# Kernel optimization log

Hardware: AMD Instinct MI355X
Metric: run time of the kernel (lower is better)

Reference implementation:

```python
import jax, jax.numpy as jnp
import numpy as np

B, S, D = 2, 2048, 1024   # batch, seq, in_shape
H, E = 16, 64             # num_heads, out_shape (per-head dim)

def setup_inputs() -> dict:
    key = jax.random.key(0)
    ks = jax.random.split(key, 5)
    x = jax.random.normal(ks[0], (B, S, D), dtype=jnp.float32)
    Wq = jax.random.normal(ks[1], (H, D, E), dtype=jnp.float32) * 0.02
    Wk = jax.random.normal(ks[2], (H, D, E), dtype=jnp.float32) * 0.02
    Wv = jax.random.normal(ks[3], (H, D, E), dtype=jnp.float32) * 0.02
    W = jax.random.normal(ks[4], (H * E, E), dtype=jnp.float32) * 0.02
    return {"x": x, "Wq": Wq, "Wk": Wk, "Wv": Wv, "W": W}

def reference(x, Wq, Wk, Wv, W):
    # Per-head projections (stacked over heads): [B,H,S,E]
    q = jnp.einsum("bsd,hde->bhse", x, Wq)
    k = jnp.einsum("bsd,hde->bhse", x, Wk)
    v = jnp.einsum("bsd,hde->bhse", x, Wv)
    scale = 1.0 / jnp.sqrt(jnp.float32(E))
    # Full causal scores [B,H,S,S] with -inf above diagonal (as in original)
    scores = jnp.einsum("bhse,bhte->bhst", q, k) * scale
    causal = jnp.tril(jnp.ones((S, S), dtype=bool))
    scores = jnp.where(causal, scores, -jnp.inf)
    attn = jax.nn.softmax(scores, axis=-1)
    ctx = jnp.einsum("bhst,bhte->bhse", attn, v)          # [B,H,S,E]
    # concat heads along last dim (head-major order matches tf.concat over list)
    ctx = jnp.transpose(ctx, (0, 2, 1, 3)).reshape(B, S, H * E)
    return ctx @ W                                         # [B,S,E]
```

## Files before the change

kernel.cpp:

```cpp
#include <hip/hip_runtime.h>
#include <hip/hip_bf16.h>
#include <cstdint>
#include <cstddef>

#define BB 2
#define SS 2048
#define DD 1024
#define HH 16
#define EE 64

typedef short bf16x8 __attribute__((ext_vector_type(8)));
typedef short s4 __attribute__((ext_vector_type(4)));
typedef float f32x4 __attribute__((ext_vector_type(4)));
typedef float float4v __attribute__((ext_vector_type(4)));
typedef unsigned int u32x2 __attribute__((ext_vector_type(2)));

#define GLDS(gp, lp) __builtin_amdgcn_global_load_lds( \
    (const __attribute__((address_space(1))) void*)(gp), \
    (__attribute__((address_space(3))) void*)(lp), 16, 0, 0)

static __device__ __forceinline__ short f2bf(float f) {
    union { float f; uint32_t u; } v; v.f = f;
    uint32_t r = (v.u + 0x7fffu + ((v.u >> 16) & 1u)) >> 16;
    return (short)r;
}

static __device__ __forceinline__ uint32_t cvtpk(float a, float b) {
    uint32_t r;
    asm("v_cvt_pk_bf16_f32 %0, %1, %2" : "=v"(r) : "v"(a), "v"(b));
    return r;
}

__global__ __launch_bounds__(256) void prep_kernel(const float* __restrict__ x,
                                                   const float* __restrict__ Wq,
                                                   const float* __restrict__ Wk,
                                                   const float* __restrict__ Wv,
                                                   const float* __restrict__ W,
                                                   short* __restrict__ xb,
                                                   short* __restrict__ wt,
                                                   short* __restrict__ wot) {
    __shared__ float tile[64][65];
    int blk = blockIdx.x;
    int t = threadIdx.x;
    if (blk < 4096) {
        int i = blk * 256 + t;
        float4v v = ((const float4v*)x)[i];
        s4 o; o[0] = f2bf(v[0]); o[1] = f2bf(v[1]); o[2] = f2bf(v[2]); o[3] = f2bf(v[3]);
        ((s4*)xb)[i] = o;
        return;
    }
    int idx = blk - 4096;
    const float* src;
    short* d;
    int R, r0;
    if (idx < 768) {
        int bx = idx & 15, by = idx >> 4;
        int which = by >> 4, mtx = by & 15;
        src = ((which == 0) ? Wq : (which == 1) ? Wk : Wv) + (size_t)mtx * DD * 64;
        d = wt + (size_t)which * HH * EE * DD + (size_t)mtx * DD * 64;
        R = DD; r0 = bx * 64;
    } else {
        int bx = idx - 768;
        src = W; d = wot; R = HH * EE; r0 = bx * 64;
    }
#pragma unroll
    for (int i = 0; i < 16; ++i) {
        int id2 = t + i * 256;
        int r = id2 >> 6, c = id2 & 63;
        tile[r][c] = src[(size_t)(r0 + r) * 64 + c];
    }
    __syncthreads();
#pragma unroll
    for (int i = 0; i < 16; ++i) {
        int id2 = t + i * 256;
        int e = id2 >> 6, dd2 = id2 & 63;
        d[(size_t)e * R + r0 + dd2] = f2bf(tile[dd2][e]);
    }
}

__global__ __launch_bounds__(256, 3) void qkv_gemm(const short* __restrict__ A,
                                                   const short* __restrict__ Bt,
                                                   short* __restrict__ Qo,
                                                   short* __restrict__ Ko,
                                                   short* __restrict__ Vto) {
    __shared__ __align__(16) short As3[3][64 * 64];
    __shared__ __align__(16) short Bs3[3][64 * 64];
    int tid = threadIdx.x;
    int wv = tid >> 6, lane = tid & 63;
    int m = lane & 15, g = lane >> 4;
    int wr = wv >> 1, wc = wv & 1;

    int xcd = blockIdx.x & 7, idx = blockIdx.x >> 3;
    int mb = (xcd & 3) * 8 + (idx & 7);
    int nb = (xcd >> 2) * 12 + (idx >> 3);
    int rowBase = mb * 128, colBase0 = nb * 128;

    int src_row[2], src_kcol[2];
#pragma unroll
    for (int j = 0; j < 2; ++j) {
        int si = j * 256 + tid;
        int sr = si >> 3, sp = si & 7;
        int sl = sp ^ (sr & 7);
        src_row[j] = 2 * sr + (sl >> 2);
        src_kcol[j] = (sl & 3) * 8;
    }
    const short* aP0 = A + (size_t)(rowBase + src_row[0]) * DD + src_kcol[0];
    const short* aP1 = A + (size_t)(rowBase + src_row[1]) * DD + src_kcol[1];
    const short* bP0 = Bt + (size_t)(colBase0 + src_row[0]) * DD + src_kcol[0];
    const short* bP1 = Bt + (size_t)(colBase0 + src_row[1]) * DD + src_kcol[1];
    int dst0 = (wv * 64) * 8;
    int dst1 = (256 + wv * 64) * 8;

    f32x4 acc[4][4];
#pragma unroll
    for (int i = 0; i < 4; ++i)
#pragma unroll
        for (int j = 0; j < 4; ++j) acc[i][j] = {0, 0, 0, 0};

    int rdoff = ((m & 1) * 64 + g * 16) ^ (((m >> 1) & 7) << 4);
    int mh = m >> 1;

    auto STAGE = [&](int buf, int kt) {
        short* ab = &As3[buf][0];
        short* bb = &Bs3[buf][0];
        GLDS(aP0 + kt, ab + dst0);
        GLDS(aP1 + kt, ab + dst1);
        GLDS(bP0 + kt, bb + dst0);
        GLDS(bP1 + kt, bb + dst1);
    };

    auto COMPUTE = [&](int buf) {
        bf16x8 af[4], bfr[4];
#pragma unroll
        for (int mi = 0; mi < 4; ++mi)
            af[mi] = *(const bf16x8*)((const char*)&As3[buf][(wr * 32 + mi * 8 + mh) * 64] + rdoff);
#pragma unroll
        for (int ni = 0; ni < 4; ++ni)
            bfr[ni] = *(const bf16x8*)((const char*)&Bs3[buf][(wc * 32 + ni * 8 + mh) * 64] + rdoff);
        asm volatile("s_waitcnt lgkmcnt(0)\ns_barrier" ::: "memory");
        __builtin_amdgcn_s_setprio(1);
#pragma unroll
        for (int mi = 0; mi < 4; ++mi)
#pragma unroll
            for (int ni = 0; ni < 4; ++ni)
                acc[mi][ni] = __builtin_amdgcn_mfma_f32_16x16x32_bf16(af[mi], bfr[ni], acc[mi][ni], 0, 0, 0);
        __builtin_amdgcn_s_setprio(0);
    };

    STAGE(0, 0);
    STAGE(1, 32);
    for (int t = 0; t < 30; ++t) {
        STAGE((t + 2) % 3, (t + 2) * 32);
        asm volatile("s_waitcnt vmcnt(8)\ns_barrier" ::: "memory");
        COMPUTE(t % 3);
    }
    asm volatile("s_waitcnt vmcnt(4)\ns_barrier" ::: "memory");
    COMPUTE(0);
    asm volatile("s_waitcnt vmcnt(0)\ns_barrier" ::: "memory");
    COMPUTE(1);

    int colw = colBase0 + wc * 64;
    int mtx = colw >> 10;
    int h = (colw >> 6) & 15;
    int rb = rowBase + wr * 64;

    if (mtx == 0) {
        const float qs = 0.125f * 1.44269504089f;
#pragma unroll
        for (int mi = 0; mi < 4; ++mi)
#pragma unroll
            for (int ni = 0; ni < 4; ++ni)
#pragma unroll
                for (int r = 0; r < 4; ++r) {
                    int row = rb + mi * 16 + g * 4 + r;
                    int b = row >> 11, s = row & 2047;
                    Qo[((size_t)(b * HH + h) * SS + s) * EE + ni * 16 + m] = f2bf(acc[mi][ni][r] * qs);
                }
    } else if (mtx == 1) {
#pragma unroll
        for (int mi = 0; mi < 4; ++mi)
#pragma unroll
            for (int ni = 0; ni < 4; ++ni)
#pragma unroll
                for (int r = 0; r < 4; ++r) {
                    int row = rb + mi * 16 + g * 4 + r;
                    int b = row >> 11, s = row & 2047;
                    Ko[((size_t)(b * HH + h) * SS + s) * EE + ni * 16 + m] = f2bf(acc[mi][ni][r]);
                }
    } else {
#pragma unroll
        for (int mi = 0; mi < 4; ++mi)
#pragma unroll
            for (int ni = 0; ni < 4; ++ni) {
                int row0 = rb + mi * 16 + g * 4;
                int b = row0 >> 11, s = row0 & 2047;
                s4 o; o[0] = f2bf(acc[mi][ni][0]); o[1] = f2bf(acc[mi][ni][1]);
                o[2] = f2bf(acc[mi][ni][2]); o[3] = f2bf(acc[mi][ni][3]);
                *(s4*)&Vto[((size_t)(b * HH + h) * EE + ni * 16 + m) * SS + s] = o;
            }
    }
}

__global__ __launch_bounds__(256, 4) void attn_kernel(const short* __restrict__ Q,
                                                      const short* __restrict__ K,
                                                      const short* __restrict__ Vt,
                                                      short* __restrict__ ctx) {
    __shared__ __align__(16) short Ks[2][64 * 64];
    __shared__ __align__(16) short Vs[2][64 * 64];
    __shared__ __align__(16) short pl[4][1024];
    int tid = threadIdx.x;
    int wv = tid >> 6, lane = tid & 63;
    int m = lane & 15, g = lane >> 4;
    int xcd = blockIdx.x & 7, i = blockIdx.x >> 3;
    int bh = xcd * 4 + (i & 3);
    int qblk = 31 - (i >> 2);
    int b = bh >> 4, h = bh & 15;
    const short* Qb = Q + (size_t)bh * SS * EE;
    const short* Kb = K + (size_t)bh * SS * EE;
    const short* Vb = Vt + (size_t)bh * EE * SS;
    int qrow = qblk * 64 + wv * 16 + m;

    int srow = wv * 8 + (lane >> 3);
    int scol_s = (((lane & 7) * 16) ^ ((srow & 7) << 4)) >> 1;

    bf16x8 qa0 = *(const bf16x8*)(Qb + (size_t)qrow * EE + g * 8);
    bf16x8 qa1 = *(const bf16x8*)(Qb + (size_t)qrow * EE + 32 + g * 8);

    int sw = (m & 7) << 4;
    int c0 = (g * 16) ^ sw;
    int c1 = (64 + g * 16) ^ sw;
    char* plrow = (char*)&pl[wv][0] + m * 128;

    float mreg = -INFINITY, lsum = 0.f;
    f32x4 o[4];
#pragma unroll
    for (int n = 0; n < 4; ++n) { o[n][0] = 0.f; o[n][1] = 0.f; o[n][2] = 0.f; o[n][3] = 0.f; }

    auto STAGE = [&](int nb, int t0) {
        short* kd = &Ks[0][0] + nb * 4096 + wv * 512;
        short* vd = &Vs[0][0] + nb * 4096 + wv * 512;
        const short* ksrc = Kb + (size_t)(t0 + srow) * EE + scol_s;
        const short* vsrc = Vb + (size_t)srow * SS + t0 + scol_s;
        GLDS(ksrc, kd);
        GLDS(ksrc + 32 * EE, kd + 2048);
        GLDS(vsrc, vd);
        GLDS(vsrc + (size_t)32 * SS, vd + 2048);
    };

    int ntile = qblk + 1;
    STAGE(0, 0);
    __syncthreads();

    for (int tt = 0; tt < ntile; ++tt) {
        if (tt + 1 < ntile) STAGE((tt + 1) & 1, (tt + 1) * 64);
        int t0 = tt * 64;
        const short* Ksb = &Ks[0][0] + (tt & 1) * 4096;
        const short* Vsb = &Vs[0][0] + (tt & 1) * 4096;

        f32x4 sc[4] = {{0,0,0,0},{0,0,0,0},{0,0,0,0},{0,0,0,0}};
#pragma unroll
        for (int n = 0; n < 4; ++n) {
            const char* krow = (const char*)(Ksb + (n * 16 + m) * 64);
            bf16x8 kb0 = *(const bf16x8*)(krow + c0);
            sc[n] = __builtin_amdgcn_mfma_f32_16x16x32_bf16(kb0, qa0, sc[n], 0, 0, 0);
            bf16x8 kb1 = *(const bf16x8*)(krow + c1);
            sc[n] = __builtin_amdgcn_mfma_f32_16x16x32_bf16(kb1, qa1, sc[n], 0, 0, 0);
        }

        if (tt == qblk) {
#pragma unroll
            for (int n = 0; n < 4; ++n)
#pragma unroll
                for (int r = 0; r < 4; ++r)
                    if (t0 + n * 16 + g * 4 + r > qrow) sc[n][r] = -INFINITY;
        }

        float mx = sc[0][0];
#pragma unroll
        for (int n = 0; n < 4; ++n)
#pragma unroll
            for (int r = 0; r < 4; ++r) mx = fmaxf(mx, sc[n][r]);
        mx = fmaxf(mx, __shfl_xor(mx, 16, 64));
        mx = fmaxf(mx, __shfl_xor(mx, 32, 64));

        if (!__all(mx <= mreg + 11.5f)) {
            float mn = fmaxf(mreg, mx);
            float al = exp2f(mreg - mn);
            lsum *= al;
#pragma unroll
            for (int n = 0; n < 4; ++n)
#pragma unroll
                for (int r = 0; r < 4; ++r) o[n][r] *= al;
            mreg = mn;
        }

#pragma unroll
        for (int n = 0; n < 4; ++n) {
            float p0 = exp2f(sc[n][0] - mreg);
            float p1 = exp2f(sc[n][1] - mreg);
            float p2 = exp2f(sc[n][2] - mreg);
            float p3 = exp2f(sc[n][3] - mreg);
            lsum += (p0 + p1) + (p2 + p3);
            u32x2 pk; pk[0] = cvtpk(p0, p1); pk[1] = cvtpk(p2, p3);
            *(u32x2*)(plrow + ((n * 32 + g * 8) ^ sw)) = pk;
        }

#pragma unroll
        for (int ks = 0; ks < 2; ++ks) {
            int cv = ks ? c1 : c0;
            bf16x8 pa = *(const bf16x8*)(plrow + cv);
#pragma unroll
            for (int n = 0; n < 4; ++n) {
                const char* vrow = (const char*)(Vsb + (n * 16 + m) * 64);
                bf16x8 vb = *(const bf16x8*)(vrow + cv);
                o[n] = __builtin_amdgcn_mfma_f32_16x16x32_bf16(vb, pa, o[n], 0, 0, 0);
            }
        }

        __syncthreads();
    }

    lsum += __shfl_xor(lsum, 16, 64);
    lsum += __shfl_xor(lsum, 32, 64);
    float inv = 1.0f / lsum;
    short* cb = ctx + (size_t)(b * SS + qrow) * (HH * EE) + h * EE;
#pragma unroll
    for (int n = 0; n < 4; ++n) {
        u32x2 k0; k0[0] = cvtpk(o[n][0] * inv, o[n][1] * inv);
        k0[1] = cvtpk(o[n][2] * inv, o[n][3] * inv);
        *(u32x2*)&cb[n * 16 + g * 4] = k0;
    }
}

__global__ __launch_bounds__(256) void outproj_kernel(const short* __restrict__ ctx,
                                                      const short* __restrict__ wot,
                                                      float* __restrict__ out) {
    __shared__ float red[4][1024];
    int wv = threadIdx.x >> 6, lane = threadIdx.x & 63;
    int m = lane & 15, g = lane >> 4;
    int r0 = blockIdx.x * 16;
    const short* arow = ctx + (size_t)(r0 + m) * (HH * EE) + g * 8;
    const short* wb = wot + g * 8;
    f32x4 acc[4] = {{0,0,0,0},{0,0,0,0},{0,0,0,0},{0,0,0,0}};
    int k0 = wv * 256;
    for (int d0 = k0; d0 < k0 + 256; d0 += 32) {
        bf16x8 a = *(const bf16x8*)(arow + d0);
#pragma unroll
        for (int n = 0; n < 4; ++n) {
            bf16x8 bbf = *(const bf16x8*)(wb + (size_t)(n * 16 + m) * (HH * EE) + d0);
            acc[n] = __builtin_amdgcn_mfma_f32_16x16x32_bf16(a, bbf, acc[n], 0, 0, 0);
        }
    }
#pragma unroll
    for (int n = 0; n < 4; ++n)
#pragma unroll
        for (int r = 0; r < 4; ++r)
            red[wv][(g * 4 + r) * 64 + n * 16 + m] = acc[n][r];
    __syncthreads();
    int t = threadIdx.x;
    float4v sum = ((const float4v*)red[0])[t];
    sum += ((const float4v*)red[1])[t];
    sum += ((const float4v*)red[2])[t];
    sum += ((const float4v*)red[3])[t];
    ((float4v*)(out + (size_t)blockIdx.x * 1024))[t] = sum;
}

extern "C" void kernel_launch(void* const* d_in, const int* in_sizes, int n_in,
                              void* d_out, int out_size, void* d_ws, size_t ws_size,
                              hipStream_t stream) {
    const float* x  = (const float*)d_in[0];
    const float* Wq = (const float*)d_in[1];
    const float* Wk = (const float*)d_in[2];
    const float* Wv = (const float*)d_in[3];
    const float* W  = (const float*)d_in[4];
    float* out = (float*)d_out;

    char* w = (char*)d_ws;
    short* xb  = (short*)w;
    short* wqt = (short*)(w + ((size_t)8 << 20));
    short* wot = wqt + (size_t)3 * HH * EE * DD;
    short* Qb  = wot + (size_t)64 * 1024;
    short* Kb  = Qb + (size_t)BB * HH * SS * EE;
    short* Vtb = Kb + (size_t)BB * HH * SS * EE;
    short* ctx = Vtb + (size_t)BB * HH * SS * EE;

    prep_kernel<<<4880, 256, 0, stream>>>(x, Wq, Wk, Wv, W, xb, wqt, wot);
    qkv_gemm<<<768, 256, 0, stream>>>(xb, wqt, Qb, Kb, Vtb);
    attn_kernel<<<1024, 256, 0, stream>>>(Qb, Kb, Vtb, ctx);
    outproj_kernel<<<256, 256, 0, stream>>>(ctx, wot, out);
}
```

Measured before the change: 94.89 us.

## Keep softmax probabilities in registers by permuting K tile row layout

```diff
diff --git a/kernel.cpp b/kernel.cpp
--- a/kernel.cpp
+++ b/kernel.cpp
@@ -14,6 +14,7 @@
 typedef float f32x4 __attribute__((ext_vector_type(4)));
 typedef float float4v __attribute__((ext_vector_type(4)));
 typedef unsigned int u32x2 __attribute__((ext_vector_type(2)));
+typedef unsigned int u32x4 __attribute__((ext_vector_type(4)));
 
 #define GLDS(gp, lp) __builtin_amdgcn_global_load_lds( \
     (const __attribute__((address_space(1))) void*)(gp), \
@@ -201,13 +202,12 @@
     }
 }
 
-__global__ __launch_bounds__(256, 4) void attn_kernel(const short* __restrict__ Q,
+__global__ __launch_bounds__(256, 5) void attn_kernel(const short* __restrict__ Q,
                                                       const short* __restrict__ K,
                                                       const short* __restrict__ Vt,
                                                       short* __restrict__ ctx) {
     __shared__ __align__(16) short Ks[2][64 * 64];
     __shared__ __align__(16) short Vs[2][64 * 64];
-    __shared__ __align__(16) short pl[4][1024];
     int tid = threadIdx.x;
     int wv = tid >> 6, lane = tid & 63;
     int m = lane & 15, g = lane >> 4;
@@ -222,6 +222,7 @@
 
     int srow = wv * 8 + (lane >> 3);
     int scol_s = (((lane & 7) * 16) ^ ((srow & 7) << 4)) >> 1;
+    int trow = ((srow >> 4) & 1) * 32 + ((srow >> 2) & 3) * 8 + (srow & 3);
 
     bf16x8 qa0 = *(const bf16x8*)(Qb + (size_t)qrow * EE + g * 8);
     bf16x8 qa1 = *(const bf16x8*)(Qb + (size_t)qrow * EE + 32 + g * 8);
@@ -229,7 +230,6 @@
     int sw = (m & 7) << 4;
     int c0 = (g * 16) ^ sw;
     int c1 = (64 + g * 16) ^ sw;
-    char* plrow = (char*)&pl[wv][0] + m * 128;
 
     float mreg = -INFINITY, lsum = 0.f;
     f32x4 o[4];
@@ -239,10 +239,10 @@
     auto STAGE = [&](int nb, int t0) {
         short* kd = &Ks[0][0] + nb * 4096 + wv * 512;
         short* vd = &Vs[0][0] + nb * 4096 + wv * 512;
-        const short* ksrc = Kb + (size_t)(t0 + srow) * EE + scol_s;
+        const short* ksrc = Kb + (size_t)(t0 + trow) * EE + scol_s;
         const short* vsrc = Vb + (size_t)srow * SS + t0 + scol_s;
         GLDS(ksrc, kd);
-        GLDS(ksrc + 32 * EE, kd + 2048);
+        GLDS(ksrc + 4 * EE, kd + 2048);
         GLDS(vsrc, vd);
         GLDS(vsrc + (size_t)32 * SS, vd + 2048);
     };
@@ -271,8 +271,10 @@
 #pragma unroll
             for (int n = 0; n < 4; ++n)
 #pragma unroll
-                for (int r = 0; r < 4; ++r)
-                    if (t0 + n * 16 + g * 4 + r > qrow) sc[n][r] = -INFINITY;
+                for (int r = 0; r < 4; ++r) {
+                    int t = t0 + 32 * (n & 1) + 8 * g + 4 * (n >> 1) + r;
+                    if (t > qrow) sc[n][r] = -INFINITY;
+                }
         }
 
         float mx = sc[0][0];
@@ -296,19 +298,22 @@
 
 #pragma unroll
         for (int n = 0; n < 4; ++n) {
-            float p0 = exp2f(sc[n][0] - mreg);
-            float p1 = exp2f(sc[n][1] - mreg);
-            float p2 = exp2f(sc[n][2] - mreg);
-            float p3 = exp2f(sc[n][3] - mreg);
-            lsum += (p0 + p1) + (p2 + p3);
-            u32x2 pk; pk[0] = cvtpk(p0, p1); pk[1] = cvtpk(p2, p3);
-            *(u32x2*)(plrow + ((n * 32 + g * 8) ^ sw)) = pk;
+            sc[n][0] = exp2f(sc[n][0] - mreg);
+            sc[n][1] = exp2f(sc[n][1] - mreg);
+            sc[n][2] = exp2f(sc[n][2] - mreg);
+            sc[n][3] = exp2f(sc[n][3] - mreg);
+            lsum += (sc[n][0] + sc[n][1]) + (sc[n][2] + sc[n][3]);
         }
 
 #pragma unroll
         for (int ks = 0; ks < 2; ++ks) {
+            union { u32x4 w; bf16x8 v; } pu;
+            pu.w[0] = cvtpk(sc[ks][0], sc[ks][1]);
+            pu.w[1] = cvtpk(sc[ks][2], sc[ks][3]);
+            pu.w[2] = cvtpk(sc[ks + 2][0], sc[ks + 2][1]);
+            pu.w[3] = cvtpk(sc[ks + 2][2], sc[ks + 2][3]);
+            bf16x8 pa = pu.v;
             int cv = ks ? c1 : c0;
-            bf16x8 pa = *(const bf16x8*)(plrow + cv);
 #pragma unroll
             for (int n = 0; n < 4; ++n) {
                 const char* vrow = (const char*)(Vsb + (n * 16 + m) * 64);
```

New measurement: 92.50 us. 1.03x faster.
